# Kernel tuning notes

Measured on AMD Instinct MI355X. Metric: run time of the kernel, lower is better.

The kernel has to match this reference:

```python
import jax, jax.numpy as jnp
import numpy as np

NEG_SLOPE = 0.2

def gatv2_layer(x, src, dst, Wl, bl, Wr, br, att, bias, N, concat):
    # Wl/Wr: [F_in, H*C]; att: [H, C]
    H, C = att.shape
    xl = (x @ Wl + bl).reshape(-1, H, C)  # source transform [N,H,C]
    xr = (x @ Wr + br).reshape(-1, H, C)  # target transform [N,H,C]
    e = jax.nn.leaky_relu(xl[src] + xr[dst], NEG_SLOPE)          # [E,H,C]
    logits = jnp.einsum('ehc,hc->eh', e, att)                    # [E,H]
    m = jax.ops.segment_max(logits, dst, num_segments=N)         # [N,H]
    p = jnp.exp(logits - m[dst])
    s = jax.ops.segment_sum(p, dst, num_segments=N)              # [N,H]
    alpha = p / s[dst]                                           # [E,H] softmax per dst
    out = jax.ops.segment_sum(alpha[:, :, None] * xl[src], dst, num_segments=N)  # [N,H,C]
    out = out.reshape(N, H * C) if concat else out.mean(axis=1)
    return out + bias


def setup_inputs() -> dict:
    key = jax.random.key(0)
    N, E, F_in = 50000, 500000, 58
    ks = jax.random.split(key, 16)
    s = 0.1
    inp = {
        'x': jax.random.normal(ks[0], (N, F_in), jnp.float32),
        'edge_index': jax.random.randint(ks[1], (2, E), 0, N, jnp.int64),
        'Wl1': jax.random.normal(ks[2], (F_in, 256), jnp.float32) * s,
        'bl1': jnp.zeros((256,), jnp.float32),
        'Wr1': jax.random.normal(ks[3], (F_in, 256), jnp.float32) * s,
        'br1': jnp.zeros((256,), jnp.float32),
        'att1': jax.random.normal(ks[4], (4, 64), jnp.float32) * s,
        'bias1': jnp.zeros((256,), jnp.float32),
        'Wl2': jax.random.normal(ks[5], (256, 256), jnp.float32) * s,
        'bl2': jnp.zeros((256,), jnp.float32),
        'Wr2': jax.random.normal(ks[6], (256, 256), jnp.float32) * s,
        'br2': jnp.zeros((256,), jnp.float32),
        'att2': jax.random.normal(ks[7], (4, 64), jnp.float32) * s,
        'bias2': jnp.zeros((256,), jnp.float32),
        'Wl3': jax.random.normal(ks[8], (256, 6), jnp.float32) * s,
        'bl3': jnp.zeros((6,), jnp.float32),
        'Wr3': jax.random.normal(ks[9], (256, 6), jnp.float32) * s,
        'br3': jnp.zeros((6,), jnp.float32),
        'att3': jax.random.normal(ks[10], (6, 1), jnp.float32) * s,
        'bias3': jnp.zeros((1,), jnp.float32),
    }
    return inp


def reference(x, edge_index, Wl1, bl1, Wr1, br1, att1, bias1,
              Wl2, bl2, Wr2, br2, att2, bias2,
              Wl3, bl3, Wr3, br3, att3, bias3):
    N = x.shape[0]
    loop = jnp.arange(N, dtype=edge_index.dtype)
    src = jnp.concatenate([edge_index[0], loop])  # self-loops (PyG default)
    dst = jnp.concatenate([edge_index[1], loop])
    h = jax.nn.elu(gatv2_layer(x, src, dst, Wl1, bl1, Wr1, br1, att1, bias1, N, True))
    h = jax.nn.elu(gatv2_layer(h, src, dst, Wl2, bl2, Wr2, br2, att2, bias2, N, True))
    out = gatv2_layer(h, src, dst, Wl3, bl3, Wr3, br3, att3, bias3, N, False)
    return out  # [N, 1]
```

## Files before the change

### kernel.cpp

```cpp
#include <hip/hip_runtime.h>
#include <math.h>

#define NEG_SLOPE 0.2f
#define LOG2E 1.4426950408889634f

typedef __attribute__((ext_vector_type(2))) _Float16 h2;
typedef __attribute__((ext_vector_type(4))) _Float16 h4;
typedef __attribute__((ext_vector_type(8))) _Float16 f16x8;
typedef __attribute__((ext_vector_type(4))) float f32x4;

typedef const __attribute__((address_space(1))) unsigned int* gu32p;
typedef __attribute__((address_space(3))) unsigned int* lu32p;

#define GLD16(g, l) __builtin_amdgcn_global_load_lds((gu32p)(g), (lu32p)(l), 16, 0, 0)

template<int CTRL>
__device__ __forceinline__ float dpp_add_f32(float x) {
    int y = __builtin_amdgcn_update_dpp(0, __float_as_int(x), CTRL, 0xF, 0xF, true);
    return x + __int_as_float(y);
}
__device__ __forceinline__ float rowsum16(float x) {
    x = dpp_add_f32<0xB1>(x);
    x = dpp_add_f32<0x4E>(x);
    x = dpp_add_f32<0x124>(x);
    x = dpp_add_f32<0x128>(x);
    return x;
}


__global__ __launch_bounds__(256) void k_count(const int* __restrict__ ei, int E, int Et,
                                               int* __restrict__ cnt) {
    int e = blockIdx.x * 256 + threadIdx.x;
    if (e < Et) {
        int d = (e < E) ? ei[E + e] : (e - E);
        atomicAdd(&cnt[d], 1);
    }
}

__global__ __launch_bounds__(256) void k_scan_block(const int* __restrict__ cnt,
                                                    int* __restrict__ out,
                                                    int* __restrict__ bsums, int n) {
    __shared__ int tmp[256];
    int t = threadIdx.x;
    int i = blockIdx.x * 256 + t;
    int v = (i < n) ? cnt[i] : 0;
    tmp[t] = v;
    __syncthreads();
    for (int d = 1; d < 256; d <<= 1) {
        int add = (t >= d) ? tmp[t - d] : 0;
        __syncthreads();
        tmp[t] += add;
        __syncthreads();
    }
    if (i < n) out[i] = tmp[t] - v;
    if (t == 255) bsums[blockIdx.x] = tmp[t];
}

__global__ __launch_bounds__(256) void k_scan_bsums(int* bsums, int nb) {
    __shared__ int tmp[256];
    int t = threadIdx.x;
    int v = (t < nb) ? bsums[t] : 0;
    tmp[t] = v;
    __syncthreads();
    for (int d = 1; d < 256; d <<= 1) {
        int add = (t >= d) ? tmp[t - d] : 0;
        __syncthreads();
        tmp[t] += add;
        __syncthreads();
    }
    if (t < nb) bsums[t] = tmp[t] - v;
}

__global__ __launch_bounds__(256) void k_scan_add(int* __restrict__ out,
                                                  const int* __restrict__ bsums,
                                                  int* __restrict__ cursor,
                                                  int n, int total) {
    int i = blockIdx.x * 256 + threadIdx.x;
    if (i < n) {
        int v = out[i] + bsums[blockIdx.x];
        out[i] = v;
        cursor[i] = v;
    }
    if (i == 0) out[n] = total;
}

__global__ __launch_bounds__(256) void k_scatter(const int* __restrict__ ei, int E, int Et,
                                                 int* __restrict__ cursor,
                                                 int* __restrict__ src_sorted) {
    int e = blockIdx.x * 256 + threadIdx.x;
    if (e < Et) {
        int s, d;
        if (e < E) { s = ei[e]; d = ei[E + e]; } else { s = d = e - E; }
        int pos = atomicAdd(&cursor[d], 1);
        src_sorted[pos] = s;
    }
}


__global__ __launch_bounds__(256) void k_cast_x(const float* __restrict__ x,
                                                _Float16* __restrict__ xb,
                                                int N, int F, int kshift) {
    int i = blockIdx.x * 256 + threadIdx.x;
    if (i < (N << kshift)) {
        int n = i >> kshift, k = i & ((1 << kshift) - 1);
        float v = (k < F) ? x[n * F + k] : 0.0f;
        xb[i] = (_Float16)v;
    }
}

__global__ __launch_bounds__(256) void k_cast_w_all(
        const float* __restrict__ Wl1, const float* __restrict__ Wr1,
        const float* __restrict__ Wl2, const float* __restrict__ Wr2,
        const float* __restrict__ Wl3, const float* __restrict__ Wr3,
        _Float16* __restrict__ wtl1, _Float16* __restrict__ wtr1,
        _Float16* __restrict__ wtl2, _Float16* __restrict__ wtr2,
        _Float16* __restrict__ w3t, int F) {
    int i = blockIdx.x * 256 + threadIdx.x;
    if (i < 32768) {
        const float* W = (i < 16384) ? Wl1 : Wr1;
        _Float16* O = (i < 16384) ? wtl1 : wtr1;
        int loc = i & 16383;
        int n = loc >> 6, k = loc & 63;
        O[loc] = (_Float16)(k < F ? W[k * 256 + n] : 0.0f);
    } else if (i < 163840) {
        int seg = i - 32768;
        const float* W = (seg < 65536) ? Wl2 : Wr2;
        _Float16* O = (seg < 65536) ? wtl2 : wtr2;
        int loc = seg & 65535;
        int n = loc >> 8, k = loc & 255;
        O[loc] = (_Float16)W[k * 256 + n];
    } else if (i < 167936) {
        int loc = i - 163840;
        int j = loc >> 8, k = loc & 255;
        float v = (j < 6) ? Wl3[k * 6 + j] : ((j < 12) ? Wr3[k * 6 + (j - 6)] : 0.0f);
        w3t[loc] = (_Float16)v;
    }
}


__global__ __launch_bounds__(256) void k_gemm_pair_mfma(
        const _Float16* __restrict__ A, int M, int Kp,
        const _Float16* __restrict__ Btl, const _Float16* __restrict__ Btr,
        const float* __restrict__ bl, const float* __restrict__ br,
        _Float16* __restrict__ Cl, _Float16* __restrict__ Cr) {
    __shared__ _Float16 As[128 * 32];
    __shared__ _Float16 Bs[128 * 32];
    const int wv = threadIdx.x >> 6, lane = threadIdx.x & 63;
    const int wr = wv >> 1, wc = wv & 1;
    const int l15 = lane & 15, l4 = lane >> 4;
    const int row0 = blockIdx.x * 128;
    const int mat  = blockIdx.y >> 1;
    const int col0 = (blockIdx.y & 1) * 128;
    const _Float16* Bt = mat ? Btr : Btl;
    const float* bias  = mat ? br  : bl;
    _Float16* C        = mat ? Cr  : Cl;

    const int rl = lane >> 2;
    const int kq = (lane & 3) * 8;
    const _Float16* ga0 = A + (size_t)min(row0 + wv * 32 + rl,      M - 1) * Kp + kq;
    const _Float16* ga1 = A + (size_t)min(row0 + wv * 32 + 16 + rl, M - 1) * Kp + kq;
    const _Float16* gb0 = Bt + (size_t)(col0 + wv * 32 + rl) * Kp + kq;
    const _Float16* gb1 = Bt + (size_t)(col0 + wv * 32 + 16 + rl) * Kp + kq;
    _Float16* la0 = &As[(wv * 32) * 32];
    _Float16* la1 = &As[(wv * 32 + 16) * 32];
    _Float16* lb0 = &Bs[(wv * 32) * 32];
    _Float16* lb1 = &Bs[(wv * 32 + 16) * 32];

    f32x4 acc[4][4];
    #pragma unroll
    for (int a = 0; a < 4; a++)
        #pragma unroll
        for (int b = 0; b < 4; b++)
            acc[a][b] = (f32x4){0.f, 0.f, 0.f, 0.f};

    for (int k0 = 0; k0 < Kp; k0 += 32) {
        GLD16(ga0 + k0, la0);
        GLD16(ga1 + k0, la1);
        GLD16(gb0 + k0, lb0);
        GLD16(gb1 + k0, lb1);
        __syncthreads();
        f16x8 wf[4], xf[4];
        #pragma unroll
        for (int ct = 0; ct < 4; ct++)
            wf[ct] = *(const f16x8*)&Bs[(wc * 64 + ct * 16 + l15) * 32 + l4 * 8];
        #pragma unroll
        for (int nt = 0; nt < 4; nt++)
            xf[nt] = *(const f16x8*)&As[(wr * 64 + nt * 16 + l15) * 32 + l4 * 8];
        #pragma unroll
        for (int ct = 0; ct < 4; ct++)
            #pragma unroll
            for (int nt = 0; nt < 4; nt++)
                acc[ct][nt] = __builtin_amdgcn_mfma_f32_16x16x32_f16(
                    wf[ct], xf[nt], acc[ct][nt], 0, 0, 0);
        __syncthreads();
    }

    float4 bv[4];
    #pragma unroll
    for (int ct = 0; ct < 4; ct++)
        bv[ct] = *(const float4*)&bias[col0 + wc * 64 + ct * 16 + l4 * 4];
    #pragma unroll
    for (int nt = 0; nt < 4; nt++) {
        int node = row0 + wr * 64 + nt * 16 + l15;
        if (node < M) {
            #pragma unroll
            for (int ct = 0; ct < 4; ct++) {
                h4 hv = {(_Float16)(acc[ct][nt][0] + bv[ct].x),
                         (_Float16)(acc[ct][nt][1] + bv[ct].y),
                         (_Float16)(acc[ct][nt][2] + bv[ct].z),
                         (_Float16)(acc[ct][nt][3] + bv[ct].w)};
                *(h4*)&C[(size_t)node * 256 + col0 + wc * 64 + ct * 16 + l4 * 4] = hv;
            }
        }
    }
}


__global__ __launch_bounds__(256) void k_gemm3_mfma(
        const _Float16* __restrict__ h,
        const _Float16* __restrict__ W3t,
        const float* __restrict__ bl, const float* __restrict__ br,
        _Float16* __restrict__ l3, int N) {
    const int wave = threadIdx.x >> 6, lane = threadIdx.x & 63;
    const int l15 = lane & 15, l4 = lane >> 4;
    const int row0 = blockIdx.x * 64 + wave * 16;
    if (row0 >= N) return;

    f16x8 bfr[8];
    #pragma unroll
    for (int ks = 0; ks < 8; ks++)
        bfr[ks] = *(const f16x8*)&W3t[l15 * 256 + ks * 32 + l4 * 8];

    const int arow = min(row0 + l15, N - 1);
    const size_t abase = (size_t)arow * 256;
    f32x4 acc = (f32x4){0.f, 0.f, 0.f, 0.f};
    #pragma unroll
    for (int ks = 0; ks < 8; ks++) {
        f16x8 af = *(const f16x8*)&h[abase + ks * 32 + l4 * 8];
        acc = __builtin_amdgcn_mfma_f32_16x16x32_f16(af, bfr[ks], acc, 0, 0, 0);
    }
    const float bv = (l15 < 6) ? bl[l15] : ((l15 < 12) ? br[l15 - 6] : 0.0f);
    #pragma unroll
    for (int r = 0; r < 4; r++) {
        int gr = row0 + l4 * 4 + r;
        if (gr < N && l15 < 12)
            l3[(size_t)gr * 16 + l15] = (_Float16)(acc[r] + bv);
    }
}


__global__ __launch_bounds__(256) void k_agg256(const _Float16* __restrict__ xl,
                                                const _Float16* __restrict__ xr,
                                                const int* __restrict__ row_ptr,
                                                const int* __restrict__ src_sorted,
                                                const float* __restrict__ att,
                                                const float* __restrict__ bias,
                                                _Float16* __restrict__ h_out, int N) {
    const int wave = threadIdx.x >> 6;
    const int lane = threadIdx.x & 63;
    const int n = __builtin_amdgcn_readfirstlane(blockIdx.x * 4 + wave);
    if (n >= N) return;
    const int ci = lane * 4;
    const h4 xr4 = *(const h4*)&xr[(size_t)n * 256 + ci];
    const float4 at4 = *(const float4*)&att[ci];
    const h2 ata = {(_Float16)(at4.x * LOG2E), (_Float16)(at4.y * LOG2E)};
    const h2 atb = {(_Float16)(at4.z * LOG2E), (_Float16)(at4.w * LOG2E)};
    float a0 = 0.f, a1 = 0.f, a2 = 0.f, a3 = 0.f;
    float m = -INFINITY, s = 0.0f;
    const int beg = row_ptr[n], end = row_ptr[n + 1];

    int j = beg;
    h4 v[8], vn[8];
    bool has = (j + 8 <= end);
    if (has) {
        #pragma unroll
        for (int e = 0; e < 8; e++) {
            int sv = src_sorted[j + e];
            v[e] = *(const h4*)&xl[(size_t)sv * 256 + ci];
        }
    }
    while (has) {
        const int jn = j + 8;
        const bool hasN = (jn + 8 <= end);
        if (hasN) {
            #pragma unroll
            for (int e = 0; e < 8; e++) {
                int sv = src_sorted[jn + e];
                vn[e] = *(const h4*)&xl[(size_t)sv * 256 + ci];
            }
        }
        float lg[8];
        #pragma unroll
        for (int e = 0; e < 8; e++) {
            h4 t = v[e] + xr4;
            h4 lk = __builtin_elementwise_max(t, t * (_Float16)NEG_SLOPE);
            h2 lo = __builtin_shufflevector(lk, lk, 0, 1);
            h2 hi = __builtin_shufflevector(lk, lk, 2, 3);
            lg[e] = __builtin_amdgcn_fdot2(lo, ata,
                        __builtin_amdgcn_fdot2(hi, atb, 0.0f, false), false);
        }
        #pragma unroll
        for (int e = 0; e < 8; e++) lg[e] = rowsum16(lg[e]);
        float bm = fmaxf(fmaxf(fmaxf(lg[0], lg[1]), fmaxf(lg[2], lg[3])),
                         fmaxf(fmaxf(lg[4], lg[5]), fmaxf(lg[6], lg[7])));
        float nm = fmaxf(m, bm);
        float sc = __builtin_amdgcn_exp2f(m - nm);
        a0 *= sc; a1 *= sc; a2 *= sc; a3 *= sc;
        float ps = 0.f;
        #pragma unroll
        for (int e = 0; e < 8; e++) {
            float p = __builtin_amdgcn_exp2f(lg[e] - nm);
            ps += p;
            a0 = fmaf(p, (float)v[e].x, a0);
            a1 = fmaf(p, (float)v[e].y, a1);
            a2 = fmaf(p, (float)v[e].z, a2);
            a3 = fmaf(p, (float)v[e].w, a3);
        }
        s = s * sc + ps;
        m = nm;
        if (hasN) {
            #pragma unroll
            for (int e = 0; e < 8; e++) v[e] = vn[e];
        }
        j = jn;
        has = hasN;
    }
    for (; j < end; j++) {
        int sv = src_sorted[j];
        h4 vv = *(const h4*)&xl[(size_t)sv * 256 + ci];
        h4 t = vv + xr4;
        h4 lk = __builtin_elementwise_max(t, t * (_Float16)NEG_SLOPE);
        h2 lo = __builtin_shufflevector(lk, lk, 0, 1);
        h2 hi = __builtin_shufflevector(lk, lk, 2, 3);
        float lg = __builtin_amdgcn_fdot2(lo, ata,
                       __builtin_amdgcn_fdot2(hi, atb, 0.0f, false), false);
        lg = rowsum16(lg);
        float nm = fmaxf(m, lg);
        float sc = __builtin_amdgcn_exp2f(m - nm);
        float p  = __builtin_amdgcn_exp2f(lg - nm);
        a0 = fmaf(p, (float)vv.x, a0 * sc);
        a1 = fmaf(p, (float)vv.y, a1 * sc);
        a2 = fmaf(p, (float)vv.z, a2 * sc);
        a3 = fmaf(p, (float)vv.w, a3 * sc);
        s = s * sc + p;
        m = nm;
    }
    const float inv = 1.0f / s;
    const float4 bv = *(const float4*)&bias[ci];
    float o0 = a0 * inv + bv.x;
    float o1 = a1 * inv + bv.y;
    float o2 = a2 * inv + bv.z;
    float o3 = a3 * inv + bv.w;
    o0 = o0 > 0.f ? o0 : (__expf(o0) - 1.f);
    o1 = o1 > 0.f ? o1 : (__expf(o1) - 1.f);
    o2 = o2 > 0.f ? o2 : (__expf(o2) - 1.f);
    o3 = o3 > 0.f ? o3 : (__expf(o3) - 1.f);
    h4 hv = {(_Float16)o0, (_Float16)o1, (_Float16)o2, (_Float16)o3};
    *(h4*)&h_out[(size_t)n * 256 + ci] = hv;
}


__global__ __launch_bounds__(64) void k_agg3(const _Float16* __restrict__ l3,
                                             const int* __restrict__ row_ptr,
                                             const int* __restrict__ src_sorted,
                                             const float* __restrict__ att3,
                                             const float* __restrict__ bias3,
                                             float* __restrict__ out, int N) {
    int n = blockIdx.x * 64 + threadIdx.x;
    if (n >= N) return;
    const h4* pn = (const h4*)&l3[(size_t)n * 16];
    h4 q1 = pn[1], q2 = pn[2];
    float xrv[6];
    xrv[0] = (float)q1.z; xrv[1] = (float)q1.w;
    xrv[2] = (float)q2.x; xrv[3] = (float)q2.y;
    xrv[4] = (float)q2.z; xrv[5] = (float)q2.w;
    float attv[6], m[6], s[6], acc[6];
    #pragma unroll
    for (int k = 0; k < 6; k++) {
        attv[k] = att3[k] * LOG2E;
        m[k] = -INFINITY; s[k] = 0.0f; acc[k] = 0.0f;
    }
    int beg = row_ptr[n], end = row_ptr[n + 1];
    for (int idx = beg; idx < end; idx++) {
        int sv = src_sorted[idx];
        const h4* ps = (const h4*)&l3[(size_t)sv * 16];
        h4 u0 = ps[0], u1 = ps[1];
        float xlv[6];
        xlv[0] = (float)u0.x; xlv[1] = (float)u0.y;
        xlv[2] = (float)u0.z; xlv[3] = (float)u0.w;
        xlv[4] = (float)u1.x; xlv[5] = (float)u1.y;
        #pragma unroll
        for (int k = 0; k < 6; k++) {
            float tt = xlv[k] + xrv[k];
            float lr = fmaxf(tt, NEG_SLOPE * tt);
            float logit = attv[k] * lr;
            float nm = fmaxf(m[k], logit);
            float sc = __builtin_amdgcn_exp2f(m[k] - nm);
            float p  = __builtin_amdgcn_exp2f(logit - nm);
            acc[k] = acc[k] * sc + p * xlv[k];
            s[k]   = s[k] * sc + p;
            m[k]   = nm;
        }
    }
    float o = 0.0f;
    #pragma unroll
    for (int k = 0; k < 6; k++) o += acc[k] / s[k];
    out[n] = o * (1.0f / 6.0f) + bias3[0];
}


extern "C" void kernel_launch(void* const* d_in, const int* in_sizes, int n_in,
                              void* d_out, int out_size, void* d_ws, size_t ws_size,
                              hipStream_t stream) {
    const float* x    = (const float*)d_in[0];
    const int*   ei   = (const int*)  d_in[1];
    const float* Wl1  = (const float*)d_in[2];
    const float* bl1  = (const float*)d_in[3];
    const float* Wr1  = (const float*)d_in[4];
    const float* br1  = (const float*)d_in[5];
    const float* att1 = (const float*)d_in[6];
    const float* bias1= (const float*)d_in[7];
    const float* Wl2  = (const float*)d_in[8];
    const float* bl2  = (const float*)d_in[9];
    const float* Wr2  = (const float*)d_in[10];
    const float* br2  = (const float*)d_in[11];
    const float* att2 = (const float*)d_in[12];
    const float* bias2= (const float*)d_in[13];
    const float* Wl3  = (const float*)d_in[14];
    const float* bl3  = (const float*)d_in[15];
    const float* Wr3  = (const float*)d_in[16];
    const float* br3  = (const float*)d_in[17];
    const float* att3 = (const float*)d_in[18];
    const float* bias3= (const float*)d_in[19];

    const int F  = in_sizes[2] / 256;
    const int N  = in_sizes[0] / F;
    const int E  = in_sizes[1] / 2;
    const int Et = E + N;

    char* ws = (char*)d_ws;
    size_t off = 0;
    auto carve = [&](size_t bytes) -> char* {
        char* p = ws + off;
        off = (off + bytes + 255) & ~(size_t)255;
        return p;
    };
    _Float16* xb   = (_Float16*)carve((size_t)N * 64 * 2);
    _Float16* xlb  = (_Float16*)carve((size_t)N * 256 * 2);
    _Float16* xrb  = (_Float16*)carve((size_t)N * 256 * 2);
    _Float16* hb   = (_Float16*)carve((size_t)N * 256 * 2);
    _Float16* wtl1 = (_Float16*)carve(256 * 64 * 2);
    _Float16* wtr1 = (_Float16*)carve(256 * 64 * 2);
    _Float16* wtl2 = (_Float16*)carve(256 * 256 * 2);
    _Float16* wtr2 = (_Float16*)carve(256 * 256 * 2);
    _Float16* w3t  = (_Float16*)carve(16 * 256 * 2);
    _Float16* l3   = (_Float16*)carve((size_t)N * 16 * 2);
    int* cnt        = (int*)carve((size_t)N * 4);
    int* row_ptr    = (int*)carve((size_t)(N + 1) * 4);
    int* cursor     = (int*)carve((size_t)N * 4);
    int* src_sorted = (int*)carve((size_t)Et * 4);
    int* bsums      = (int*)carve(1024 * 4);

    const int gN  = (N + 255) / 256;
    const int gEt = (Et + 255) / 256;
    const int gW  = (N + 3) / 4;

    hipMemsetAsync(cnt, 0, (size_t)N * 4, stream);
    k_count<<<gEt, 256, 0, stream>>>(ei, E, Et, cnt);
    k_scan_block<<<gN, 256, 0, stream>>>(cnt, row_ptr, bsums, N);
    k_scan_bsums<<<1, 256, 0, stream>>>(bsums, gN);
    k_scan_add<<<gN, 256, 0, stream>>>(row_ptr, bsums, cursor, N, Et);
    k_scatter<<<gEt, 256, 0, stream>>>(ei, E, Et, cursor, src_sorted);

    k_cast_x<<<((N << 6) + 255) / 256, 256, 0, stream>>>(x, xb, N, F, 6);
    k_cast_w_all<<<656, 256, 0, stream>>>(Wl1, Wr1, Wl2, Wr2, Wl3, Wr3,
                                          wtl1, wtr1, wtl2, wtr2, w3t, F);

    dim3 gemm_grid((N + 127) / 128, 4);

    k_gemm_pair_mfma<<<gemm_grid, 256, 0, stream>>>(xb, N, 64, wtl1, wtr1, bl1, br1, xlb, xrb);
    k_agg256<<<gW, 256, 0, stream>>>(xlb, xrb, row_ptr, src_sorted, att1, bias1, hb, N);

    k_gemm_pair_mfma<<<gemm_grid, 256, 0, stream>>>(hb, N, 256, wtl2, wtr2, bl2, br2, xlb, xrb);
    k_agg256<<<gW, 256, 0, stream>>>(xlb, xrb, row_ptr, src_sorted, att2, bias2, hb, N);

    k_gemm3_mfma<<<(N + 63) / 64, 256, 0, stream>>>(hb, w3t, bl3, br3, l3, N);
    k_agg3<<<(N + 63) / 64, 64, 0, stream>>>(l3, row_ptr, src_sorted, att3, bias3,
                                             (float*)d_out, N);
}
```

Baseline: 334.4 us.

## Fuse prep kernels, double-buffer GEMM LDS, ping-pong aggregation loads

Merges the edge-count, x-cast and weight-cast kernels into one launch, split by block-index ranges, to cut launch overhead. The MFMA GEMM gets double-buffered LDS so the next K-slice is staged while the current one is computed, dropping one barrier per iteration. The aggregation loop swaps the copy-based prefetch for two alternating register buffers, which avoids register moves. Costs are twice the GEMM LDS and possible occupancy or register pressure changes.

```diff
diff --git a/kernel.cpp b/kernel.cpp
--- a/kernel.cpp
+++ b/kernel.cpp
@@ -27,15 +27,6 @@
     return x;
 }
 
-
-__global__ __launch_bounds__(256) void k_count(const int* __restrict__ ei, int E, int Et,
-                                               int* __restrict__ cnt) {
-    int e = blockIdx.x * 256 + threadIdx.x;
-    if (e < Et) {
-        int d = (e < E) ? ei[E + e] : (e - E);
-        atomicAdd(&cnt[d], 1);
-    }
-}
 
 __global__ __launch_bounds__(256) void k_scan_block(const int* __restrict__ cnt,
                                                     int* __restrict__ out,
@@ -97,43 +88,49 @@
 }
 
 
-__global__ __launch_bounds__(256) void k_cast_x(const float* __restrict__ x,
-                                                _Float16* __restrict__ xb,
-                                                int N, int F, int kshift) {
-    int i = blockIdx.x * 256 + threadIdx.x;
-    if (i < (N << kshift)) {
-        int n = i >> kshift, k = i & ((1 << kshift) - 1);
-        float v = (k < F) ? x[n * F + k] : 0.0f;
-        xb[i] = (_Float16)v;
-    }
-}
-
-__global__ __launch_bounds__(256) void k_cast_w_all(
+__global__ __launch_bounds__(256) void k_prep(
+        const int* __restrict__ ei, int E, int Et, int* __restrict__ cnt,
+        const float* __restrict__ x, _Float16* __restrict__ xb, int N, int F,
         const float* __restrict__ Wl1, const float* __restrict__ Wr1,
         const float* __restrict__ Wl2, const float* __restrict__ Wr2,
         const float* __restrict__ Wl3, const float* __restrict__ Wr3,
         _Float16* __restrict__ wtl1, _Float16* __restrict__ wtr1,
         _Float16* __restrict__ wtl2, _Float16* __restrict__ wtr2,
-        _Float16* __restrict__ w3t, int F) {
-    int i = blockIdx.x * 256 + threadIdx.x;
-    if (i < 32768) {
-        const float* W = (i < 16384) ? Wl1 : Wr1;
-        _Float16* O = (i < 16384) ? wtl1 : wtr1;
-        int loc = i & 16383;
-        int n = loc >> 6, k = loc & 63;
-        O[loc] = (_Float16)(k < F ? W[k * 256 + n] : 0.0f);
-    } else if (i < 163840) {
-        int seg = i - 32768;
-        const float* W = (seg < 65536) ? Wl2 : Wr2;
-        _Float16* O = (seg < 65536) ? wtl2 : wtr2;
-        int loc = seg & 65535;
-        int n = loc >> 8, k = loc & 255;
-        O[loc] = (_Float16)W[k * 256 + n];
-    } else if (i < 167936) {
-        int loc = i - 163840;
-        int j = loc >> 8, k = loc & 255;
-        float v = (j < 6) ? Wl3[k * 6 + j] : ((j < 12) ? Wr3[k * 6 + (j - 6)] : 0.0f);
-        w3t[loc] = (_Float16)v;
+        _Float16* __restrict__ w3t, int gEt, int gX) {
+    const int b = blockIdx.x;
+    if (b < gEt) {
+        int e = b * 256 + threadIdx.x;
+        if (e < Et) {
+            int d = (e < E) ? ei[E + e] : (e - E);
+            atomicAdd(&cnt[d], 1);
+        }
+    } else if (b < gEt + gX) {
+        int i = (b - gEt) * 256 + threadIdx.x;
+        if (i < (N << 6)) {
+            int n = i >> 6, k = i & 63;
+            xb[i] = (_Float16)(k < F ? x[n * F + k] : 0.0f);
+        }
+    } else {
+        int i = (b - gEt - gX) * 256 + threadIdx.x;
+        if (i < 32768) {
+            const float* W = (i < 16384) ? Wl1 : Wr1;
+            _Float16* O = (i < 16384) ? wtl1 : wtr1;
+            int loc = i & 16383;
+            int n = loc >> 6, k = loc & 63;
+            O[loc] = (_Float16)(k < F ? W[k * 256 + n] : 0.0f);
+        } else if (i < 163840) {
+            int seg = i - 32768;
+            const float* W = (seg < 65536) ? Wl2 : Wr2;
+            _Float16* O = (seg < 65536) ? wtl2 : wtr2;
+            int loc = seg & 65535;
+            int n = loc >> 8, k = loc & 255;
+            O[loc] = (_Float16)W[k * 256 + n];
+        } else if (i < 167936) {
+            int loc = i - 163840;
+            int j = loc >> 8, k = loc & 255;
+            float v = (j < 6) ? Wl3[k * 6 + j] : ((j < 12) ? Wr3[k * 6 + (j - 6)] : 0.0f);
+            w3t[loc] = (_Float16)v;
+        }
     }
 }
 
@@ -143,8 +140,8 @@
         const _Float16* __restrict__ Btl, const _Float16* __restrict__ Btr,
         const float* __restrict__ bl, const float* __restrict__ br,
         _Float16* __restrict__ Cl, _Float16* __restrict__ Cr) {
-    __shared__ _Float16 As[128 * 32];
-    __shared__ _Float16 Bs[128 * 32];
+    __shared__ _Float16 As[2][128 * 32];
+    __shared__ _Float16 Bs[2][128 * 32];
     const int wv = threadIdx.x >> 6, lane = threadIdx.x & 63;
     const int wr = wv >> 1, wc = wv & 1;
     const int l15 = lane & 15, l4 = lane >> 4;
@@ -161,10 +158,6 @@
     const _Float16* ga1 = A + (size_t)min(row0 + wv * 32 + 16 + rl, M - 1) * Kp + kq;
     const _Float16* gb0 = Bt + (size_t)(col0 + wv * 32 + rl) * Kp + kq;
     const _Float16* gb1 = Bt + (size_t)(col0 + wv * 32 + 16 + rl) * Kp + kq;
-    _Float16* la0 = &As[(wv * 32) * 32];
-    _Float16* la1 = &As[(wv * 32 + 16) * 32];
-    _Float16* lb0 = &Bs[(wv * 32) * 32];
-    _Float16* lb1 = &Bs[(wv * 32 + 16) * 32];
 
     f32x4 acc[4][4];
     #pragma unroll
@@ -173,26 +166,32 @@
         for (int b = 0; b < 4; b++)
             acc[a][b] = (f32x4){0.f, 0.f, 0.f, 0.f};
 
-    for (int k0 = 0; k0 < Kp; k0 += 32) {
-        GLD16(ga0 + k0, la0);
-        GLD16(ga1 + k0, la1);
-        GLD16(gb0 + k0, lb0);
-        GLD16(gb1 + k0, lb1);
+    auto stage = [&](int k0, int b) {
+        GLD16(ga0 + k0, &As[b][(wv * 32) * 32]);
+        GLD16(ga1 + k0, &As[b][(wv * 32 + 16) * 32]);
+        GLD16(gb0 + k0, &Bs[b][(wv * 32) * 32]);
+        GLD16(gb1 + k0, &Bs[b][(wv * 32 + 16) * 32]);
+    };
+
+    const int nsteps = Kp >> 5;
+    stage(0, 0);
+    for (int s = 0; s < nsteps; s++) {
         __syncthreads();
+        if (s + 1 < nsteps) stage((s + 1) * 32, (s + 1) & 1);
+        const int b = s & 1;
         f16x8 wf[4], xf[4];
         #pragma unroll
         for (int ct = 0; ct < 4; ct++)
-            wf[ct] = *(const f16x8*)&Bs[(wc * 64 + ct * 16 + l15) * 32 + l4 * 8];
+            wf[ct] = *(const f16x8*)&Bs[b][(wc * 64 + ct * 16 + l15) * 32 + l4 * 8];
         #pragma unroll
         for (int nt = 0; nt < 4; nt++)
-            xf[nt] = *(const f16x8*)&As[(wr * 64 + nt * 16 + l15) * 32 + l4 * 8];
+            xf[nt] = *(const f16x8*)&As[b][(wr * 64 + nt * 16 + l15) * 32 + l4 * 8];
         #pragma unroll
         for (int ct = 0; ct < 4; ct++)
             #pragma unroll
             for (int nt = 0; nt < 4; nt++)
                 acc[ct][nt] = __builtin_amdgcn_mfma_f32_16x16x32_f16(
                     wf[ct], xf[nt], acc[ct][nt], 0, 0, 0);
-        __syncthreads();
     }
 
     float4 bv[4];
@@ -269,26 +268,15 @@
     float m = -INFINITY, s = 0.0f;
     const int beg = row_ptr[n], end = row_ptr[n + 1];
 
-    int j = beg;
-    h4 v[8], vn[8];
-    bool has = (j + 8 <= end);
-    if (has) {
+    h4 va[8], vb[8];
+    auto load8 = [&](h4 (&v)[8], int jj) {
         #pragma unroll
         for (int e = 0; e < 8; e++) {
-            int sv = src_sorted[j + e];
+            int sv = src_sorted[jj + e];
             v[e] = *(const h4*)&xl[(size_t)sv * 256 + ci];
         }
-    }
-    while (has) {
-        const int jn = j + 8;
-        const bool hasN = (jn + 8 <= end);
-        if (hasN) {
-            #pragma unroll
-            for (int e = 0; e < 8; e++) {
-                int sv = src_sorted[jn + e];
-                vn[e] = *(const h4*)&xl[(size_t)sv * 256 + ci];
-            }
-        }
+    };
+    auto proc8 = [&](const h4 (&v)[8]) {
         float lg[8];
         #pragma unroll
         for (int e = 0; e < 8; e++) {
@@ -318,12 +306,22 @@
         }
         s = s * sc + ps;
         m = nm;
-        if (hasN) {
-            #pragma unroll
-            for (int e = 0; e < 8; e++) v[e] = vn[e];
-        }
-        j = jn;
-        has = hasN;
+    };
+
+    int j = beg;
+    bool hasA = (j + 8 <= end);
+    if (hasA) load8(va, j);
+    while (hasA) {
+        const int j1 = j + 8;
+        const bool hasB = (j1 + 8 <= end);
+        if (hasB) load8(vb, j1);
+        proc8(va);
+        if (!hasB) { j = j1; break; }
+        const int j2 = j1 + 8;
+        hasA = (j2 + 8 <= end);
+        if (hasA) load8(va, j2);
+        proc8(vb);
+        j = j2;
     }
     for (; j < end; j++) {
         int sv = src_sorted[j];
@@ -463,19 +461,19 @@
 
     const int gN  = (N + 255) / 256;
     const int gEt = (Et + 255) / 256;
+    const int gX  = ((N << 6) + 255) / 256;
     const int gW  = (N + 3) / 4;
 
     hipMemsetAsync(cnt, 0, (size_t)N * 4, stream);
-    k_count<<<gEt, 256, 0, stream>>>(ei, E, Et, cnt);
+    k_prep<<<gEt + gX + 656, 256, 0, stream>>>(ei, E, Et, cnt, x, xb, N, F,
+                                               Wl1, Wr1, Wl2, Wr2, Wl3, Wr3,
+                                               wtl1, wtr1, wtl2, wtr2, w3t, gEt, gX);
+
     k_scan_block<<<gN, 256, 0, stream>>>(cnt, row_ptr, bsums, N);
     k_scan_bsums<<<1, 256, 0, stream>>>(bsums, gN);
     k_scan_add<<<gN, 256, 0, stream>>>(row_ptr, bsums, cursor, N, Et);
     k_scatter<<<gEt, 256, 0, stream>>>(ei, E, Et, cursor, src_sorted);
 
-    k_cast_x<<<((N << 6) + 255) / 256, 256, 0, stream>>>(x, xb, N, F, 6);
-    k_cast_w_all<<<656, 256, 0, stream>>>(Wl1, Wr1, Wl2, Wr2, Wl3, Wr3,
-                                          wtl1, wtr1, wtl2, wtr2, w3t, F);
-
     dim3 gemm_grid((N + 127) / 128, 4);
 
     k_gemm_pair_mfma<<<gemm_grid, 256, 0, stream>>>(xb, N, 64, wtl1, wtr1, bl1, br1, xlb, xrb);
```

Result: slower. 346.0 us (+3.5%).
